# Kernel tuning notes

Hardware: AMD Instinct MI355X
Metric: run time of the kernel (lower is better)

The kernel has to match this reference:

```python
import jax, jax.numpy as jnp
import numpy as np

NU, NI, D, L = 100_000, 150_000, 64, 3
N = NU + NI
NNZ_A, NNZ_S = 2_000_000, 800_000


def _spmm(rows, cols, vals, X, n):
    # sparse [n, m] @ X[m, D] via gather + segment-sum (COO)
    return jax.ops.segment_sum(vals[:, None] * X[cols], rows, num_segments=n)


def _bilinear(x, c, W, b):
    # nn.Bilinear(D, D, 1) with second arg a single broadcast vector c: x_n^T W c + b
    return x @ (W @ c) + b[0]  # [Nu]


def setup_inputs() -> dict:
    key = jax.random.key(0)
    ks = jax.random.split(key, 20)
    f = jnp.float32
    inp = {
        "u1": jax.random.normal(ks[0], (NU, D), f) * 0.1,
        "u2": jax.random.normal(ks[1], (NU, D), f) * 0.1,
        "item_emb": jax.random.normal(ks[2], (NI, D), f) * 0.1,
        "Wi": jax.random.normal(ks[3], (D, D), f) * (1.0 / np.sqrt(D)),
        "Wc": jax.random.normal(ks[4], (D, D), f) * (1.0 / np.sqrt(D)),
        "Ws": jax.random.normal(ks[5], (D, 2 * D), f) * (1.0 / np.sqrt(2 * D)),
        "fk_W": jax.random.normal(ks[6], (D, D), f) * (1.0 / np.sqrt(D)),
        "fk_b": jax.random.normal(ks[7], (1,), f) * 0.01,
        "A_vals": jax.random.uniform(ks[8], (NNZ_A,), f) * 0.2,
        "A2_vals": jax.random.uniform(ks[9], (NNZ_A,), f) * 0.2,
        "S_vals": jax.random.uniform(ks[10], (NNZ_S,), f) * 0.2,
        "A_rows": jax.random.randint(ks[11], (NNZ_A,), 0, N, jnp.int32),
        "A_cols": jax.random.randint(ks[12], (NNZ_A,), 0, N, jnp.int32),
        "A2_rows": jax.random.randint(ks[13], (NNZ_A,), 0, N, jnp.int32),
        "A2_cols": jax.random.randint(ks[14], (NNZ_A,), 0, N, jnp.int32),
        "S_rows": jax.random.randint(ks[15], (NNZ_S,), 0, NU, jnp.int32),
        "S_cols": jax.random.randint(ks[16], (NNZ_S,), 0, NU, jnp.int32),
        "shuffle1": jax.random.permutation(ks[17], NU).astype(jnp.int32),
        "shuffle2": jax.random.permutation(ks[18], NU).astype(jnp.int32),
    }
    return inp


def reference(u1, u2, item_emb, Wi, Wc, Ws, fk_W, fk_b,
              A_vals, A2_vals, S_vals,
              A_rows, A_cols, A2_rows, A2_cols, S_rows, S_cols,
              shuffle1, shuffle2):
    # CLDS.computer, epoch >= 2000 branch. S1 = S2 = socialGraph2 in the source.
    users_emb0 = (u1 + u2) * 0.5
    all_emb = jnp.concatenate([users_emb0, item_emb])  # [N, D]
    u1_neg = u1[shuffle1]
    u2_neg = u2[shuffle2]
    embs = [all_emb]
    logits_true, logits_false = [], []
    for layer in range(L):
        rows, cols, vals = (A_rows, A_cols, A_vals) if layer == 0 else (A2_rows, A2_cols, A2_vals)
        agg = _spmm(rows, cols, vals, all_emb, N)          # [N, D]
        u_int, items_next = agg[:NU], agg[NU:]
        u_next = jnp.tanh(u_int @ Wi.T)                     # social_i + tanh
        all_emb = jnp.concatenate([u_next, items_next])
        u1_soc = jnp.tanh(_spmm(S_rows, S_cols, S_vals, u1, NU) @ Wc.T)
        u2_soc = jnp.tanh(_spmm(S_rows, S_cols, S_vals, u2, NU) @ Wc.T)
        u1_neg = jnp.tanh(_spmm(S_rows, S_cols, S_vals, u1_neg, NU) @ Wc.T)
        u2_neg = jnp.tanh(_spmm(S_rows, S_cols, S_vals, u2_neg, NU) @ Wc.T)
        c1 = jnp.mean(u1_soc, axis=0)
        c2 = jnp.mean(u2_soc, axis=0)
        sc1 = _bilinear(u2_soc, c1, fk_W, fk_b)
        sc2 = _bilinear(u1_soc, c2, fk_W, fk_b)
        sc3 = _bilinear(u2_neg, c1, fk_W, fk_b)
        sc4 = _bilinear(u1_neg, c2, fk_W, fk_b)
        logits_true.append(jnp.concatenate([sc1, sc2]))     # [2*NU]
        logits_false.append(jnp.concatenate([sc3, sc4]))
        u_comb = (u1_soc + u2_soc) * 0.5
        users = jnp.concatenate([u_next, u_comb], axis=1) @ Ws.T
        users = users / jnp.linalg.norm(users)              # global L2 norm, as in torch .norm(2)
        embs.append(jnp.concatenate([users, items_next]))
    final = jnp.mean(jnp.stack(embs, axis=1), axis=1)       # [N, D]
    # torch: stack([1,2Nu] x 2L, dim=2) -> [1,2Nu,2L] -> view(1,-1)
    logits = jnp.stack(logits_true + logits_false, axis=1).reshape(1, -1)
    return final[:NU], final[NU:], logits
```

## Files before the change

kernel.cpp:

```cpp
#include <hip/hip_runtime.h>

#define NU 100000
#define NI 150000
#define NTOT 250000
#define DD 64
#define NNZ_A 2000000
#define NNZ_S 800000
#define SCAN_CHUNK 2048

typedef unsigned int uint;
typedef unsigned short ushort;

#define LB __launch_bounds__(256, 4)

#define RDLANE_F(x, k) __uint_as_float(__builtin_amdgcn_readlane(__float_as_uint(x), (unsigned)(k)))
#define RDLANE_I(x, k) ((int)__builtin_amdgcn_readlane((unsigned)(x), (unsigned)(k)))

__device__ __forceinline__ uint f2bf_bits(float x) {
  uint a = __float_as_uint(x);
  return (a + 0x7fffu + ((a >> 16) & 1u)) >> 16;
}
__device__ __forceinline__ ushort f2bf(float x) { return (ushort)f2bf_bits(x); }
__device__ __forceinline__ float bf2f(ushort h) { return __uint_as_float(((uint)h) << 16); }
__device__ __forceinline__ uint pack_bf16x2(float lo, float hi) {
  return f2bf_bits(lo) | (f2bf_bits(hi) << 16);
}
__device__ __forceinline__ float unpk_lo(uint p) { return __uint_as_float(p << 16); }
__device__ __forceinline__ float unpk_hi(uint p) { return __uint_as_float(p & 0xffff0000u); }

__device__ __forceinline__ void gemm64x2_lds(float aA, float aB,
                                             const float* __restrict__ Wt, int lane,
                                             float& oA, float& oB) {
  oA = 0.f; oB = 0.f;
#pragma unroll 16
  for (int k = 0; k < 64; ++k) {
    float wk = Wt[k * 65 + lane];
    oA = fmaf(RDLANE_F(aA, k), wk, oA);
    oB = fmaf(RDLANE_F(aB, k), wk, oB);
  }
}

__device__ __forceinline__ void stage_wt(const float* __restrict__ W, float* __restrict__ Wt) {
  for (int idx = threadIdx.x; idx < 64 * 64; idx += blockDim.x)
    Wt[(idx & 63) * 65 + (idx >> 6)] = W[idx];
  __syncthreads();
}

__global__ void k_init(const float* __restrict__ u1, const float* __restrict__ u2,
                       const float* __restrict__ item, ushort* __restrict__ emb_bf,
                       float* __restrict__ out_final) {
  int idx = blockIdx.x * blockDim.x + threadIdx.x;
  const int tot = NTOT * DD;
  const int nu = NU * DD;
  for (; idx < tot; idx += gridDim.x * blockDim.x) {
    float v;
    if (idx < nu) v = 0.5f * (u1[idx] + u2[idx]);
    else          v = item[idx - nu];
    emb_bf[idx] = f2bf(v);
    out_final[idx] = v;
  }
}

__global__ void k_hist_rank(const int* __restrict__ rows, int* __restrict__ cnt,
                            int* __restrict__ rank, int nnz) {
  int tid = blockIdx.x * blockDim.x + threadIdx.x;
  int gsz = gridDim.x * blockDim.x;
  for (int b = tid; b < nnz; b += gsz * 8) {
#pragma unroll
    for (int u = 0; u < 8; ++u) {
      int i = b + u * gsz;
      if (i < nnz) rank[i] = atomicAdd(&cnt[rows[i]], 1);
    }
  }
}

__global__ void k_scan1(const int* __restrict__ cnt, int* __restrict__ bsum, int n) {
  __shared__ int sdata[256];
  int base = blockIdx.x * SCAN_CHUNK;
  int s = 0;
#pragma unroll
  for (int k = 0; k < 8; ++k) {
    int i = base + threadIdx.x * 8 + k;
    s += (i < n) ? cnt[i] : 0;
  }
  sdata[threadIdx.x] = s;
  __syncthreads();
  for (int off = 128; off > 0; off >>= 1) {
    if (threadIdx.x < off) sdata[threadIdx.x] += sdata[threadIdx.x + off];
    __syncthreads();
  }
  if (threadIdx.x == 0) bsum[blockIdx.x] = sdata[0];
}

__global__ void k_scan2(int* bsum, int nb) {
  __shared__ int sdata[256];
  int v = (threadIdx.x < nb) ? bsum[threadIdx.x] : 0;
  sdata[threadIdx.x] = v;
  __syncthreads();
  for (int off = 1; off < 256; off <<= 1) {
    int t = (threadIdx.x >= (unsigned)off) ? sdata[threadIdx.x - off] : 0;
    __syncthreads();
    sdata[threadIdx.x] += t;
    __syncthreads();
  }
  if (threadIdx.x < nb) bsum[threadIdx.x] = sdata[threadIdx.x] - v;
}

__global__ void k_scan3(const int* __restrict__ cnt, const int* __restrict__ bsum,
                        int* __restrict__ rowptr, int n, int nnz) {
  __shared__ int sdata[256];
  int base = blockIdx.x * SCAN_CHUNK;
  int loc[8];
  int s = 0;
#pragma unroll
  for (int k = 0; k < 8; ++k) {
    int i = base + threadIdx.x * 8 + k;
    loc[k] = (i < n) ? cnt[i] : 0;
    s += loc[k];
  }
  sdata[threadIdx.x] = s;
  __syncthreads();
  for (int off = 1; off < 256; off <<= 1) {
    int t = (threadIdx.x >= (unsigned)off) ? sdata[threadIdx.x - off] : 0;
    __syncthreads();
    sdata[threadIdx.x] += t;
    __syncthreads();
  }
  int pre = bsum[blockIdx.x] + sdata[threadIdx.x] - s;
#pragma unroll
  for (int k = 0; k < 8; ++k) {
    int i = base + threadIdx.x * 8 + k;
    if (i < n) { rowptr[i] = pre; pre += loc[k]; }
  }
  if (blockIdx.x == 0 && threadIdx.x == 0) rowptr[n] = nnz;
}

__global__ void k_scatter2(const int* __restrict__ rows, const int* __restrict__ cols,
                           const float* __restrict__ vals, const int* __restrict__ ptr,
                           const int* __restrict__ rank, int2* __restrict__ cv, int nnz) {
  int tid = blockIdx.x * blockDim.x + threadIdx.x;
  int gsz = gridDim.x * blockDim.x;
  for (int b = tid; b < nnz; b += gsz * 8) {
#pragma unroll
    for (int u = 0; u < 8; ++u) {
      int i = b + u * gsz;
      if (i < nnz) {
        int r = rows[i];
        cv[ptr[r] + rank[i]] = make_int2(cols[i], __float_as_int(vals[i]));
      }
    }
  }
}

__global__ LB void k_transform(const float* __restrict__ u1, const float* __restrict__ u2,
                               const float* __restrict__ Wc, uint* __restrict__ SOCPt) {
  __shared__ float Wt[64 * 65];
  stage_wt(Wc, Wt);
  int lane = threadIdx.x & 63;
  int wid = (blockIdx.x * blockDim.x + threadIdx.x) >> 6;
  int nw = (gridDim.x * blockDim.x) >> 6;
  for (int i = wid; i < NU; i += nw) {
    float a1 = u1[(size_t)i * DD + lane];
    float a2 = u2[(size_t)i * DD + lane];
    float o1, o2;
    gemm64x2_lds(a1, a2, Wt, lane, o1, o2);
    SOCPt[(size_t)i * DD + lane] = pack_bf16x2(o1, o2);
  }
}

__global__ void k_negmap(const uint* __restrict__ SOCPt, const int* __restrict__ s1,
                         const int* __restrict__ s2, uint2* __restrict__ QUADP) {
  int idx = blockIdx.x * blockDim.x + threadIdx.x;
  const int tot = NU * DD;
  for (; idx < tot; idx += gridDim.x * blockDim.x) {
    int i = idx >> 6, j = idx & 63;
    uint soc = SOCPt[idx];
    uint lo = SOCPt[(size_t)s1[i] * DD + j];
    uint hi = SOCPt[(size_t)s2[i] * DD + j];
    QUADP[idx] = make_uint2(soc, (lo & 0xffffu) | (hi & 0xffff0000u));
  }
}

__global__ LB void k_quadS(const int* __restrict__ rowptr, const int2* __restrict__ cv,
                           const uint2* __restrict__ QUADP, const float* __restrict__ Wc,
                           ushort* __restrict__ u1s, ushort* __restrict__ u2s,
                           ushort* __restrict__ n1o, ushort* __restrict__ n2o,
                           uint* __restrict__ NEGPa) {
  __shared__ float Wt[64 * 65];
  stage_wt(Wc, Wt);
  int lane = threadIdx.x & 63;
  int wid = (blockIdx.x * blockDim.x + threadIdx.x) >> 6;
  int nw = (gridDim.x * blockDim.x) >> 6;
  for (int r = wid; r < NU; r += nw) {
    int start = rowptr[r], end = rowptr[r + 1];
    float a1 = 0.f, a2 = 0.f, a3 = 0.f, a4 = 0.f;
    for (int p0 = start; p0 < end; p0 += 64) {
      int n = min(64, end - p0);
      int2 e = cv[p0 + (lane < n ? lane : 0)];
      for (int k = 0; k < n; k += 8) {
        uint2 q[8];
        float vv[8];
#pragma unroll
        for (int u = 0; u < 8; ++u) {
          int kk = k + u;
          int ks = min(kk, n - 1);
          int c = RDLANE_I(e.x, ks);
          vv[u] = (kk < n) ? RDLANE_F(__int_as_float(e.y), ks) : 0.f;
          q[u] = QUADP[(size_t)c * DD + lane];
        }
#pragma unroll
        for (int u = 0; u < 8; ++u) {
          a1 = fmaf(vv[u], unpk_lo(q[u].x), a1);
          a2 = fmaf(vv[u], unpk_hi(q[u].x), a2);
          a3 = fmaf(vv[u], unpk_lo(q[u].y), a3);
          a4 = fmaf(vv[u], unpk_hi(q[u].y), a4);
        }
      }
    }
    float t1 = tanhf(a1), t2 = tanhf(a2), t3 = tanhf(a3), t4 = tanhf(a4);
    u1s[(size_t)r * DD + lane] = f2bf(t1);
    u2s[(size_t)r * DD + lane] = f2bf(t2);
    n1o[(size_t)r * DD + lane] = f2bf(t3);
    n2o[(size_t)r * DD + lane] = f2bf(t4);
    float o3, o4;
    gemm64x2_lds(t3, t4, Wt, lane, o3, o4);
    NEGPa[(size_t)r * DD + lane] = pack_bf16x2(o3, o4);
  }
}

__global__ LB void k_dualS(const int* __restrict__ rowptr, const int2* __restrict__ cv,
                           const uint* __restrict__ T, const float* __restrict__ Wc,
                           const float* __restrict__ wva, const float* __restrict__ wvb,
                           const float* __restrict__ fkb, float* __restrict__ out_logits,
                           int slot, uint* __restrict__ Tnext) {
  __shared__ float Wt[64 * 65];
  stage_wt(Wc, Wt);
  int lane = threadIdx.x & 63;
  int wid = (blockIdx.x * blockDim.x + threadIdx.x) >> 6;
  int nw = (gridDim.x * blockDim.x) >> 6;
  float b = fkb[0];
  float wa = wva[lane], wb = wvb[lane];
  for (int r = wid; r < NU; r += nw) {
    int start = rowptr[r], end = rowptr[r + 1];
    float accA = 0.f, accB = 0.f;
    for (int p0 = start; p0 < end; p0 += 64) {
      int n = min(64, end - p0);
      int2 e = cv[p0 + (lane < n ? lane : 0)];
      for (int k = 0; k < n; k += 8) {
        uint q[8];
        float vv[8];
#pragma unroll
        for (int u = 0; u < 8; ++u) {
          int kk = k + u;
          int ks = min(kk, n - 1);
          int c = RDLANE_I(e.x, ks);
          vv[u] = (kk < n) ? RDLANE_F(__int_as_float(e.y), ks) : 0.f;
          q[u] = T[(size_t)c * DD + lane];
        }
#pragma unroll
        for (int u = 0; u < 8; ++u) {
          accA = fmaf(vv[u], unpk_lo(q[u]), accA);
          accB = fmaf(vv[u], unpk_hi(q[u]), accB);
        }
      }
    }
    float ta = tanhf(accA), tb = tanhf(accB);
    float pa = ta * wa, pb = tb * wb;
#pragma unroll
    for (int off = 32; off > 0; off >>= 1) {
      pa += __shfl_xor(pa, off);
      pb += __shfl_xor(pb, off);
    }
    if (lane == 0) {
      out_logits[(size_t)(NU + r) * 6 + slot] = pa + b;
      out_logits[(size_t)r * 6 + slot] = pb + b;
    }
    if (Tnext) {
      float oa, ob;
      gemm64x2_lds(ta, tb, Wt, lane, oa, ob);
      Tnext[(size_t)r * DD + lane] = pack_bf16x2(oa, ob);
    }
  }
}

__global__ LB void k_spmm_fusedA2(const int* __restrict__ rowptr, const int2* __restrict__ cv,
                                  const ushort* __restrict__ X, const float* __restrict__ W,
                                  ushort* __restrict__ embNext, float* __restrict__ outF) {
  __shared__ float Wt[64 * 65];
  stage_wt(W, Wt);
  int lane = threadIdx.x & 63;
  int wid = (blockIdx.x * blockDim.x + threadIdx.x) >> 6;
  int nw = (gridDim.x * blockDim.x) >> 6;
  for (int r = wid * 2; r < NTOT; r += nw * 2) {
    int sA = rowptr[r], m = rowptr[r + 1], eB = rowptr[r + 2];
    float accA = 0.f, accB = 0.f;
    for (int pA = sA, pB = m; pA < m || pB < eB; pA += 64, pB += 64) {
      int nA = (pA < m) ? min(64, m - pA) : 0;
      int nB = (pB < eB) ? min(64, eB - pB) : 0;
      int2 eAv = cv[(nA ? pA : 0) + (lane < nA ? lane : 0)];
      int2 eBv = cv[(nB ? pB : 0) + (lane < nB ? lane : 0)];
      int kmax = max(nA, nB);
      for (int k = 0; k < kmax; k += 8) {
        uint hA[8], hB[8];
        float vA[8], vB[8];
#pragma unroll
        for (int u = 0; u < 8; ++u) {
          int kk = k + u;
          int ksA = min(kk, max(nA - 1, 0));
          int ksB = min(kk, max(nB - 1, 0));
          int cA = RDLANE_I(eAv.x, ksA);
          int cB = RDLANE_I(eBv.x, ksB);
          vA[u] = (kk < nA) ? RDLANE_F(__int_as_float(eAv.y), ksA) : 0.f;
          vB[u] = (kk < nB) ? RDLANE_F(__int_as_float(eBv.y), ksB) : 0.f;
          hA[u] = X[(size_t)cA * DD + lane];
          hB[u] = X[(size_t)cB * DD + lane];
        }
#pragma unroll
        for (int u = 0; u < 8; ++u) {
          accA = fmaf(vA[u], __uint_as_float(hA[u] << 16), accA);
          accB = fmaf(vB[u], __uint_as_float(hB[u] << 16), accB);
        }
      }
    }
    if (r < NU) {
      float oA, oB;
      gemm64x2_lds(accA, accB, Wt, lane, oA, oB);
      embNext[(size_t)r * DD + lane] = f2bf(tanhf(oA));
      embNext[(size_t)(r + 1) * DD + lane] = f2bf(tanhf(oB));
    } else {
      embNext[(size_t)r * DD + lane] = f2bf(accA);
      embNext[(size_t)(r + 1) * DD + lane] = f2bf(accB);
      outF[(size_t)r * DD + lane] += accA;
      outF[(size_t)(r + 1) * DD + lane] += accB;
    }
  }
}

__global__ void k_colsum2(const ushort* __restrict__ x1, const ushort* __restrict__ x2,
                          float* __restrict__ c1, float* __restrict__ c2) {
  int lane = threadIdx.x & 63;
  int wid = (blockIdx.x * blockDim.x + threadIdx.x) >> 6;
  int nw = (gridDim.x * blockDim.x) >> 6;
  float a1 = 0.f, a2 = 0.f;
  for (int i = wid; i < NU; i += nw) {
    a1 += bf2f(x1[(size_t)i * DD + lane]);
    a2 += bf2f(x2[(size_t)i * DD + lane]);
  }
  atomicAdd(&c1[lane], a1);
  atomicAdd(&c2[lane], a2);
}

__global__ void k_wvec(const float* __restrict__ fkW, const float* __restrict__ c1r,
                       const float* __restrict__ c2r, float* __restrict__ w1,
                       float* __restrict__ w2) {
  int j = threadIdx.x;
  float a1 = 0.f, a2 = 0.f;
  for (int k = 0; k < 64; ++k) {
    float w = fkW[j * 64 + k];
    a1 += w * c1r[k];
    a2 += w * c2r[k];
  }
  w1[j] = a1 * (1.0f / NU);
  w2[j] = a2 * (1.0f / NU);
}

__global__ void k_logits4(const ushort* __restrict__ u1s, const ushort* __restrict__ u2s,
                          const ushort* __restrict__ n1o, const ushort* __restrict__ n2o,
                          const float* __restrict__ w1, const float* __restrict__ w2,
                          const float* __restrict__ fkb, float* __restrict__ out_logits) {
  int lane = threadIdx.x & 63;
  int wid = (blockIdx.x * blockDim.x + threadIdx.x) >> 6;
  int nw = (gridDim.x * blockDim.x) >> 6;
  float b = fkb[0];
  for (int i = wid; i < 2 * NU; i += nw) {
    bool lo = i < NU;
    int r = lo ? i : i - NU;
    const ushort* xs = lo ? u2s : u1s;
    const ushort* xn = lo ? n2o : n1o;
    const float* wv = lo ? w1 : w2;
    float wvl = wv[lane];
    float ps = bf2f(xs[(size_t)r * DD + lane]) * wvl;
    float pn = bf2f(xn[(size_t)r * DD + lane]) * wvl;
#pragma unroll
    for (int off = 32; off > 0; off >>= 1) {
      ps += __shfl_xor(ps, off);
      pn += __shfl_xor(pn, off);
    }
    if (lane == 0) {
      float vs = ps + b;
      out_logits[(size_t)i * 6 + 0] = vs;
      out_logits[(size_t)i * 6 + 1] = vs;
      out_logits[(size_t)i * 6 + 2] = vs;
      out_logits[(size_t)i * 6 + 3] = pn + b;
    }
  }
}

__global__ LB void k_comb_gemm(const ushort* __restrict__ u1s, const ushort* __restrict__ u2s,
                               const float* __restrict__ Ws, ushort* __restrict__ UC) {
  __shared__ float Wt[64 * 65];
  for (int idx = threadIdx.x; idx < 64 * 64; idx += blockDim.x)
    Wt[(idx & 63) * 65 + (idx >> 6)] = Ws[(idx >> 6) * 128 + 64 + (idx & 63)];
  __syncthreads();
  int lane = threadIdx.x & 63;
  int wid = (blockIdx.x * blockDim.x + threadIdx.x) >> 6;
  int nw = (gridDim.x * blockDim.x) >> 6;
  for (int i = wid; i < NU; i += nw) {
    float c = 0.5f * (bf2f(u1s[(size_t)i * DD + lane]) + bf2f(u2s[(size_t)i * DD + lane]));
    float o = 0.f;
#pragma unroll 16
    for (int k = 0; k < 64; ++k)
      o = fmaf(RDLANE_F(c, k), Wt[k * 65 + lane], o);
    UC[(size_t)i * DD + lane] = f2bf(o);
  }
}

__global__ LB void k_users(const ushort* __restrict__ u_next, const ushort* __restrict__ uc,
                           const float* __restrict__ Ws, float* __restrict__ users_raw,
                           float* __restrict__ sumsq) {
  __shared__ float Wt[64 * 65];
  for (int idx = threadIdx.x; idx < 64 * 64; idx += blockDim.x)
    Wt[(idx & 63) * 65 + (idx >> 6)] = Ws[(idx >> 6) * 128 + (idx & 63)];
  __syncthreads();
  int lane = threadIdx.x & 63;
  int wid = (blockIdx.x * blockDim.x + threadIdx.x) >> 6;
  int nw = (gridDim.x * blockDim.x) >> 6;
  float ss = 0.f;
  for (int i = wid; i < NU; i += nw) {
    float va = bf2f(u_next[(size_t)i * DD + lane]);
    float acc = bf2f(uc[(size_t)i * DD + lane]);
#pragma unroll 16
    for (int k = 0; k < 64; ++k)
      acc = fmaf(RDLANE_F(va, k), Wt[k * 65 + lane], acc);
    users_raw[(size_t)i * DD + lane] = acc;
    ss += acc * acc;
  }
#pragma unroll
  for (int off = 32; off > 0; off >>= 1) ss += __shfl_xor(ss, off);
  if (lane == 0) atomicAdd(sumsq, ss);
}

__global__ void k_users_acc(const float* __restrict__ users_raw,
                            const float* __restrict__ sumsq, float* __restrict__ out_final) {
  float scale = 1.0f / sqrtf(*sumsq);
  int idx = blockIdx.x * blockDim.x + threadIdx.x;
  for (; idx < NU * DD; idx += gridDim.x * blockDim.x)
    out_final[idx] += users_raw[idx] * scale;
}

__global__ void k_scale(float* __restrict__ out_final) {
  int idx = blockIdx.x * blockDim.x + threadIdx.x;
  const int tot = NTOT * DD;
  for (; idx < tot; idx += gridDim.x * blockDim.x) out_final[idx] *= 0.25f;
}

extern "C" void kernel_launch(void* const* d_in, const int* in_sizes, int n_in,
                              void* d_out, int out_size, void* d_ws, size_t ws_size,
                              hipStream_t stream) {
  const float* u1      = (const float*)d_in[0];
  const float* u2      = (const float*)d_in[1];
  const float* item    = (const float*)d_in[2];
  const float* Wi      = (const float*)d_in[3];
  const float* Wc      = (const float*)d_in[4];
  const float* Ws      = (const float*)d_in[5];
  const float* fk_W    = (const float*)d_in[6];
  const float* fk_b    = (const float*)d_in[7];
  const float* A_vals  = (const float*)d_in[8];
  const float* A2_vals = (const float*)d_in[9];
  const float* S_vals  = (const float*)d_in[10];
  const int*   A_rows  = (const int*)d_in[11];
  const int*   A_cols  = (const int*)d_in[12];
  const int*   A2_rows = (const int*)d_in[13];
  const int*   A2_cols = (const int*)d_in[14];
  const int*   S_rows  = (const int*)d_in[15];
  const int*   S_cols  = (const int*)d_in[16];
  const int*   sh1     = (const int*)d_in[17];
  const int*   sh2     = (const int*)d_in[18];

  float* ws = (float*)d_ws;
  ushort* embA_bf = (ushort*)ws;
  ushort* embB_bf = (ushort*)(ws + 8000000);
  uint2*  QUADP   = (uint2*)(ws + 16000000);
  uint*   NEGPb   = (uint*)(ws + 16000000);
  float*  uraw    = ws + 22400000;
  uint*   NEGPa   = (uint*)(ws + 28800000);
  ushort* u1s     = (ushort*)(ws + 35200000);
  ushort* u2s     = (ushort*)(ws + 38400000);
  int2*   cvA2    = (int2*)(ws + 35200000);
  int*    ptrA2   = (int*)(ws + 39200000);
  uint*   SOCPt   = (uint*)(ws + 41600000);
  ushort* n1o     = (ushort*)(ws + 41600000);
  ushort* UCb     = (ushort*)(ws + 41600000);
  ushort* n2o     = (ushort*)(ws + 44800000);
  int2*   cvA     = (int2*)(ws + 48000000);
  int2*   cvS     = (int2*)(ws + 52000000);
  int*    ptrA    = (int*)(ws + 53600000);
  int*    ptrS    = ptrA + (NTOT + 1);
  int*    cnt     = ptrS + (NU + 1);
  int*    bsum    = cnt + NTOT;
  float*  c1r     = (float*)(bsum + 256);
  float*  c2r     = c1r + 64;
  float*  w1      = c2r + 64;
  float*  w2      = w1 + 64;
  float*  sumsq   = w2 + 64;
  int*    rank    = (int*)(ws + 54200520);

  float* out        = (float*)d_out;
  float* out_logits = out + (size_t)NTOT * DD;

  auto build = [&](const int* rows, const int* cols, const float* vals,
                   int n, int nnz, int* ptr, int2* cv) {
    int nb = (n + SCAN_CHUNK - 1) / SCAN_CHUNK;
    int gb = (nnz + 2047) / 2048;
    hipMemsetAsync(cnt, 0, (size_t)n * sizeof(int), stream);
    k_hist_rank<<<gb, 256, 0, stream>>>(rows, cnt, rank, nnz);
    k_scan1<<<nb, 256, 0, stream>>>(cnt, bsum, n);
    k_scan2<<<1, 256, 0, stream>>>(bsum, nb);
    k_scan3<<<nb, 256, 0, stream>>>(cnt, bsum, ptr, n, nnz);
    k_scatter2<<<gb, 256, 0, stream>>>(rows, cols, vals, ptr, rank, cv, nnz);
  };

  build(S_rows, S_cols, S_vals, NU, NNZ_S, ptrS, cvS);
  build(A_rows, A_cols, A_vals, NTOT, NNZ_A, ptrA, cvA);

  hipMemsetAsync(c1r, 0, 128 * sizeof(float), stream);
  k_init<<<2048, 256, 0, stream>>>(u1, u2, item, embA_bf, out);
  k_transform<<<1024, 256, 0, stream>>>(u1, u2, Wc, SOCPt);
  k_negmap<<<1024, 256, 0, stream>>>(SOCPt, sh1, sh2, QUADP);

  k_quadS<<<2048, 256, 0, stream>>>(ptrS, cvS, QUADP, Wc,
                                    u1s, u2s, n1o, n2o, NEGPa);
  k_colsum2<<<256, 256, 0, stream>>>(u1s, u2s, c1r, c2r);
  k_wvec<<<1, 64, 0, stream>>>(fk_W, c1r, c2r, w1, w2);
  k_logits4<<<1024, 256, 0, stream>>>(u1s, u2s, n1o, n2o, w1, w2, fk_b, out_logits);
  k_comb_gemm<<<1024, 256, 0, stream>>>(u1s, u2s, Ws, UCb);

  build(A2_rows, A2_cols, A2_vals, NTOT, NNZ_A, ptrA2, cvA2);

  ushort* embCur = embA_bf;
  ushort* embNext = embB_bf;
  for (int l = 0; l < 3; ++l) {
    const int* pA = (l == 0) ? ptrA : ptrA2;
    const int2* cA = (l == 0) ? cvA : cvA2;

    k_spmm_fusedA2<<<4096, 256, 0, stream>>>(pA, cA, embCur, Wi, embNext, out);

    if (l == 1)
      k_dualS<<<2048, 256, 0, stream>>>(ptrS, cvS, NEGPa, Wc, w2, w1, fk_b,
                                        out_logits, 4, NEGPb);
    else if (l == 2)
      k_dualS<<<2048, 256, 0, stream>>>(ptrS, cvS, NEGPb, Wc, w2, w1, fk_b,
                                        out_logits, 5, (uint*)nullptr);

    hipMemsetAsync(sumsq, 0, sizeof(float), stream);
    k_users<<<1024, 256, 0, stream>>>(embNext, UCb, Ws, uraw, sumsq);
    k_users_acc<<<2048, 256, 0, stream>>>(uraw, sumsq, out);

    { ushort* t = embCur; embCur = embNext; embNext = t; }
  }

  k_scale<<<2048, 256, 0, stream>>>(out);
}
```

Measured before the change: 1.688 ms.

## Fold final scaling into producers, split SpMM full/tail chunks, use fast tanh

The final 0.25 scale pass is removed by applying 0.25 at init, at the item accumulation and in the user normalisation scale, which saves one full read-modify-write over the output. The gather loops in the social and A-SpMM kernels are split into a fast path for full 8-entry groups without clamping, plus a masked tail, and use 32-bit index arithmetic. The interleaved two-row A-SpMM loop is replaced by processing the two rows one after the other. tanhf is replaced with an exp-based approximation, which risks small accuracy differences and overflow handling for large inputs.

```diff
diff --git a/kernel.cpp b/kernel.cpp
--- a/kernel.cpp
+++ b/kernel.cpp
@@ -27,6 +27,11 @@
 }
 __device__ __forceinline__ float unpk_lo(uint p) { return __uint_as_float(p << 16); }
 __device__ __forceinline__ float unpk_hi(uint p) { return __uint_as_float(p & 0xffff0000u); }
+
+__device__ __forceinline__ float tanh_fast(float x) {
+  float e = __expf(2.0f * x);
+  return 1.0f - __fdividef(2.0f, e + 1.0f);
+}
 
 __device__ __forceinline__ void gemm64x2_lds(float aA, float aB,
                                              const float* __restrict__ Wt, int lane,
@@ -38,6 +43,15 @@
     oA = fmaf(RDLANE_F(aA, k), wk, oA);
     oB = fmaf(RDLANE_F(aB, k), wk, oB);
   }
+}
+
+__device__ __forceinline__ float gemm64x1_lds(float a, const float* __restrict__ Wt,
+                                              int lane) {
+  float s = 0.f;
+#pragma unroll 16
+  for (int k = 0; k < 64; ++k)
+    s = fmaf(RDLANE_F(a, k), Wt[k * 65 + lane], s);
+  return s;
 }
 
 __device__ __forceinline__ void stage_wt(const float* __restrict__ W, float* __restrict__ Wt) {
@@ -57,7 +71,7 @@
     if (idx < nu) v = 0.5f * (u1[idx] + u2[idx]);
     else          v = item[idx - nu];
     emb_bf[idx] = f2bf(v);
-    out_final[idx] = v;
+    out_final[idx] = 0.25f * v;
   }
 }
 
@@ -197,7 +211,26 @@
     for (int p0 = start; p0 < end; p0 += 64) {
       int n = min(64, end - p0);
       int2 e = cv[p0 + (lane < n ? lane : 0)];
-      for (int k = 0; k < n; k += 8) {
+      int nfull = n & ~7;
+      int k = 0;
+      for (; k < nfull; k += 8) {
+        uint2 q[8];
+        float vv[8];
+#pragma unroll
+        for (int u = 0; u < 8; ++u) {
+          int c = RDLANE_I(e.x, k + u);
+          vv[u] = RDLANE_F(__int_as_float(e.y), k + u);
+          q[u] = QUADP[(uint)c * 64u + (uint)lane];
+        }
+#pragma unroll
+        for (int u = 0; u < 8; ++u) {
+          a1 = fmaf(vv[u], unpk_lo(q[u].x), a1);
+          a2 = fmaf(vv[u], unpk_hi(q[u].x), a2);
+          a3 = fmaf(vv[u], unpk_lo(q[u].y), a3);
+          a4 = fmaf(vv[u], unpk_hi(q[u].y), a4);
+        }
+      }
+      if (k < n) {
         uint2 q[8];
         float vv[8];
 #pragma unroll
@@ -206,7 +239,7 @@
           int ks = min(kk, n - 1);
           int c = RDLANE_I(e.x, ks);
           vv[u] = (kk < n) ? RDLANE_F(__int_as_float(e.y), ks) : 0.f;
-          q[u] = QUADP[(size_t)c * DD + lane];
+          q[u] = QUADP[(uint)c * 64u + (uint)lane];
         }
 #pragma unroll
         for (int u = 0; u < 8; ++u) {
@@ -217,7 +250,7 @@
         }
       }
     }
-    float t1 = tanhf(a1), t2 = tanhf(a2), t3 = tanhf(a3), t4 = tanhf(a4);
+    float t1 = tanh_fast(a1), t2 = tanh_fast(a2), t3 = tanh_fast(a3), t4 = tanh_fast(a4);
     u1s[(size_t)r * DD + lane] = f2bf(t1);
     u2s[(size_t)r * DD + lane] = f2bf(t2);
     n1o[(size_t)r * DD + lane] = f2bf(t3);
@@ -246,7 +279,24 @@
     for (int p0 = start; p0 < end; p0 += 64) {
       int n = min(64, end - p0);
       int2 e = cv[p0 + (lane < n ? lane : 0)];
-      for (int k = 0; k < n; k += 8) {
+      int nfull = n & ~7;
+      int k = 0;
+      for (; k < nfull; k += 8) {
+        uint q[8];
+        float vv[8];
+#pragma unroll
+        for (int u = 0; u < 8; ++u) {
+          int c = RDLANE_I(e.x, k + u);
+          vv[u] = RDLANE_F(__int_as_float(e.y), k + u);
+          q[u] = T[(uint)c * 64u + (uint)lane];
+        }
+#pragma unroll
+        for (int u = 0; u < 8; ++u) {
+          accA = fmaf(vv[u], unpk_lo(q[u]), accA);
+          accB = fmaf(vv[u], unpk_hi(q[u]), accB);
+        }
+      }
+      if (k < n) {
         uint q[8];
         float vv[8];
 #pragma unroll
@@ -255,7 +305,7 @@
           int ks = min(kk, n - 1);
           int c = RDLANE_I(e.x, ks);
           vv[u] = (kk < n) ? RDLANE_F(__int_as_float(e.y), ks) : 0.f;
-          q[u] = T[(size_t)c * DD + lane];
+          q[u] = T[(uint)c * 64u + (uint)lane];
         }
 #pragma unroll
         for (int u = 0; u < 8; ++u) {
@@ -264,7 +314,7 @@
         }
       }
     }
-    float ta = tanhf(accA), tb = tanhf(accB);
+    float ta = tanh_fast(accA), tb = tanh_fast(accB);
     float pa = ta * wa, pb = tb * wb;
 #pragma unroll
     for (int off = 32; off > 0; off >>= 1) {
@@ -292,46 +342,57 @@
   int wid = (blockIdx.x * blockDim.x + threadIdx.x) >> 6;
   int nw = (gridDim.x * blockDim.x) >> 6;
   for (int r = wid * 2; r < NTOT; r += nw * 2) {
-    int sA = rowptr[r], m = rowptr[r + 1], eB = rowptr[r + 2];
-    float accA = 0.f, accB = 0.f;
-    for (int pA = sA, pB = m; pA < m || pB < eB; pA += 64, pB += 64) {
-      int nA = (pA < m) ? min(64, m - pA) : 0;
-      int nB = (pB < eB) ? min(64, eB - pB) : 0;
-      int2 eAv = cv[(nA ? pA : 0) + (lane < nA ? lane : 0)];
-      int2 eBv = cv[(nB ? pB : 0) + (lane < nB ? lane : 0)];
-      int kmax = max(nA, nB);
-      for (int k = 0; k < kmax; k += 8) {
-        uint hA[8], hB[8];
-        float vA[8], vB[8];
-#pragma unroll
-        for (int u = 0; u < 8; ++u) {
-          int kk = k + u;
-          int ksA = min(kk, max(nA - 1, 0));
-          int ksB = min(kk, max(nB - 1, 0));
-          int cA = RDLANE_I(eAv.x, ksA);
-          int cB = RDLANE_I(eBv.x, ksB);
-          vA[u] = (kk < nA) ? RDLANE_F(__int_as_float(eAv.y), ksA) : 0.f;
-          vB[u] = (kk < nB) ? RDLANE_F(__int_as_float(eBv.y), ksB) : 0.f;
-          hA[u] = X[(size_t)cA * DD + lane];
-          hB[u] = X[(size_t)cB * DD + lane];
-        }
-#pragma unroll
-        for (int u = 0; u < 8; ++u) {
-          accA = fmaf(vA[u], __uint_as_float(hA[u] << 16), accA);
-          accB = fmaf(vB[u], __uint_as_float(hB[u] << 16), accB);
+    float acc0 = 0.f, acc1 = 0.f;
+#pragma unroll
+    for (int rr = 0; rr < 2; ++rr) {
+      int rs = rowptr[r + rr], re = rowptr[r + rr + 1];
+      float a = 0.f;
+      for (int p0 = rs; p0 < re; p0 += 64) {
+        int n = min(64, re - p0);
+        int2 e = cv[p0 + (lane < n ? lane : 0)];
+        int nfull = n & ~7;
+        int k = 0;
+        for (; k < nfull; k += 8) {
+          uint h[8];
+          float vv[8];
+#pragma unroll
+          for (int u = 0; u < 8; ++u) {
+            int c = RDLANE_I(e.x, k + u);
+            vv[u] = RDLANE_F(__int_as_float(e.y), k + u);
+            h[u] = X[(uint)c * 64u + (uint)lane];
+          }
+#pragma unroll
+          for (int u = 0; u < 8; ++u)
+            a = fmaf(vv[u], __uint_as_float(h[u] << 16), a);
+        }
+        if (k < n) {
+          uint h[8];
+          float vv[8];
+#pragma unroll
+          for (int u = 0; u < 8; ++u) {
+            int kk = k + u;
+            int ks = min(kk, n - 1);
+            int c = RDLANE_I(e.x, ks);
+            vv[u] = (kk < n) ? RDLANE_F(__int_as_float(e.y), ks) : 0.f;
+            h[u] = X[(uint)c * 64u + (uint)lane];
+          }
+#pragma unroll
+          for (int u = 0; u < 8; ++u)
+            a = fmaf(vv[u], __uint_as_float(h[u] << 16), a);
         }
       }
+      if (rr == 0) acc0 = a; else acc1 = a;
     }
     if (r < NU) {
       float oA, oB;
-      gemm64x2_lds(accA, accB, Wt, lane, oA, oB);
-      embNext[(size_t)r * DD + lane] = f2bf(tanhf(oA));
-      embNext[(size_t)(r + 1) * DD + lane] = f2bf(tanhf(oB));
+      gemm64x2_lds(acc0, acc1, Wt, lane, oA, oB);
+      embNext[(size_t)r * DD + lane] = f2bf(tanh_fast(oA));
+      embNext[(size_t)(r + 1) * DD + lane] = f2bf(tanh_fast(oB));
     } else {
-      embNext[(size_t)r * DD + lane] = f2bf(accA);
-      embNext[(size_t)(r + 1) * DD + lane] = f2bf(accB);
-      outF[(size_t)r * DD + lane] += accA;
-      outF[(size_t)(r + 1) * DD + lane] += accB;
+      embNext[(size_t)r * DD + lane] = f2bf(acc0);
+      embNext[(size_t)(r + 1) * DD + lane] = f2bf(acc1);
+      outF[(size_t)r * DD + lane] += 0.25f * acc0;
+      outF[(size_t)(r + 1) * DD + lane] += 0.25f * acc1;
     }
   }
 }
@@ -407,11 +468,7 @@
   int nw = (gridDim.x * blockDim.x) >> 6;
   for (int i = wid; i < NU; i += nw) {
     float c = 0.5f * (bf2f(u1s[(size_t)i * DD + lane]) + bf2f(u2s[(size_t)i * DD + lane]));
-    float o = 0.f;
-#pragma unroll 16
-    for (int k = 0; k < 64; ++k)
-      o = fmaf(RDLANE_F(c, k), Wt[k * 65 + lane], o);
-    UC[(size_t)i * DD + lane] = f2bf(o);
+    UC[(size_t)i * DD + lane] = f2bf(gemm64x1_lds(c, Wt, lane));
   }
 }
 
@@ -428,10 +485,7 @@
   float ss = 0.f;
   for (int i = wid; i < NU; i += nw) {
     float va = bf2f(u_next[(size_t)i * DD + lane]);
-    float acc = bf2f(uc[(size_t)i * DD + lane]);
-#pragma unroll 16
-    for (int k = 0; k < 64; ++k)
-      acc = fmaf(RDLANE_F(va, k), Wt[k * 65 + lane], acc);
+    float acc = bf2f(uc[(size_t)i * DD + lane]) + gemm64x1_lds(va, Wt, lane);
     users_raw[(size_t)i * DD + lane] = acc;
     ss += acc * acc;
   }
@@ -442,16 +496,10 @@
 
 __global__ void k_users_acc(const float* __restrict__ users_raw,
                             const float* __restrict__ sumsq, float* __restrict__ out_final) {
-  float scale = 1.0f / sqrtf(*sumsq);
+  float scale = 0.25f / sqrtf(*sumsq);
   int idx = blockIdx.x * blockDim.x + threadIdx.x;
   for (; idx < NU * DD; idx += gridDim.x * blockDim.x)
     out_final[idx] += users_raw[idx] * scale;
-}
-
-__global__ void k_scale(float* __restrict__ out_final) {
-  int idx = blockIdx.x * blockDim.x + threadIdx.x;
-  const int tot = NTOT * DD;
-  for (; idx < tot; idx += gridDim.x * blockDim.x) out_final[idx] *= 0.25f;
 }
 
 extern "C" void kernel_launch(void* const* d_in, const int* in_sizes, int n_in,
@@ -558,6 +606,4 @@
 
     { ushort* t = embCur; embCur = embNext; embNext = t; }
   }
-
-  k_scale<<<2048, 256, 0, stream>>>(out);
-}
+}
```

Result: faster. 1.652 ms (-2.1%).
